# Performance work log

Measured on AMD Instinct MI355X. Metric: run time of the kernel, lower is better.

The kernel has to match this reference:

```python
import jax, jax.numpy as jnp
import numpy as np

N, E, D, L, G = 100000, 3200000, 64, 4, 512
BN_EPS = 1e-5


def setup_inputs() -> dict:
    key = jax.random.key(0)
    ks = jax.random.split(key, 6)
    x = jax.random.normal(ks[0], (N, D), dtype=jnp.float32)
    edge_index = jax.random.randint(ks[1], (2, E), 0, N, dtype=jnp.int64)
    batch = jnp.sort(jax.random.randint(ks[2], (N,), 0, G, dtype=jnp.int64))
    scale = 1.0 / np.sqrt(D).astype(np.float32)
    W1 = jax.random.normal(ks[3], (L, D, D), dtype=jnp.float32) * scale
    b1 = jnp.zeros((L, D), dtype=jnp.float32)
    W2 = jax.random.normal(ks[4], (L, D, D), dtype=jnp.float32) * scale
    b2 = jnp.zeros((L, D), dtype=jnp.float32)
    gamma = jnp.ones((L, D), dtype=jnp.float32)
    beta = jnp.zeros((L, D), dtype=jnp.float32)
    return {"x": x, "W1": W1, "b1": b1, "W2": W2, "b2": b2,
            "gamma": gamma, "beta": beta,
            "edge_index": edge_index, "batch": batch}


def reference(x, W1, b1, W2, b2, gamma, beta, edge_index, batch):
    src, dst = edge_index[0], edge_index[1]
    # in-degree for mean aggregation (flow source_to_target: gather x[src], scatter at dst)
    deg = jax.ops.segment_sum(jnp.ones((E,), x.dtype), dst, num_segments=N)
    inv_deg = jnp.where(deg > 0, 1.0 / jnp.maximum(deg, 1.0), 0.0)[:, None]
    # per-graph node counts for global_mean_pool
    gcnt = jax.ops.segment_sum(jnp.ones((N,), x.dtype), batch, num_segments=G)
    inv_gcnt = jnp.where(gcnt > 0, 1.0 / jnp.maximum(gcnt, 1.0), 0.0)[:, None]

    h = x
    node_pool = jnp.zeros((N, D), x.dtype)
    g_pool = jnp.zeros((G, D), x.dtype)
    for l in range(L):
        # GINConv(aggr='mean', eps=0): nn(x + mean_{j in N(i)} x_j)
        agg = jax.ops.segment_sum(h[src], dst, num_segments=N) * inv_deg
        z = h + agg
        z = jnp.maximum(z @ W1[l] + b1[l], 0.0) @ W2[l] + b2[l]  # Linear-ReLU-Linear
        z = jnp.maximum(z, 0.0)  # outer F.relu
        # BatchNorm1d (training-mode batch statistics over node dim)
        mu = z.mean(axis=0)
        var = z.var(axis=0)
        h = (z - mu) * jax.lax.rsqrt(var + BN_EPS) * gamma[l] + beta[l]
        node_pool = node_pool + h
        g_pool = g_pool + jax.ops.segment_sum(h, batch, num_segments=G) * inv_gcnt
    return node_pool, g_pool
```

## Files before the change

### kernel.cpp

```cpp
#include <hip/hip_runtime.h>
#include <hip/hip_bf16.h>


typedef unsigned short ushort_t;
typedef unsigned int uint_t;
typedef __attribute__((ext_vector_type(8))) short bf16x8;
typedef __attribute__((ext_vector_type(4))) float f32x4;

#define NN 100000
#define EE 3200000
#define GG 512
#define NBK 391
#define NHB 256
#define ECHUNK 12500
#define MLPBLOCKS 782
#define NWAVE (MLPBLOCKS * 4)
#define YSTRIDE 68

__global__ __launch_bounds__(256) void detect_kernel(
    const uint_t* __restrict__ xw, const uint_t* __restrict__ ew,
    const uint_t* __restrict__ bw, int* __restrict__ flags)
{
    __shared__ int sb[256], se[256], sbb[256];
    int t = threadIdx.x;
    uint_t w = xw[t];
    uint_t eL = (w >> 7) & 0xffu;
    sb[t] = (eL >= 112u && eL <= 135u) ? 1 : 0;
    se[t] = (ew[2 * t + 1] == 0u) ? 1 : 0;
    sbb[t] = (bw[NN - 512 + 2 * t + 1] == 0u) ? 1 : 0;
    __syncthreads();
    for (int off = 128; off > 0; off >>= 1) {
        if (t < off) { sb[t] += sb[t + off]; se[t] += se[t + off]; sbb[t] += sbb[t + off]; }
        __syncthreads();
    }
    if (t == 0) {
        flags[0] = (sb[0] < 128) ? 1 : 0;
        flags[1] = (se[0] >= 128) ? 1 : 0;
        flags[2] = (sbb[0] >= 128) ? 1 : 0;
    }
}

__global__ __launch_bounds__(256) void cvt_w_kernel(
    const void* __restrict__ W1, const void* __restrict__ b1,
    const void* __restrict__ W2, const void* __restrict__ b2,
    const void* __restrict__ g, const void* __restrict__ be,
    const int* __restrict__ flags, ushort_t* __restrict__ wp,
    float* __restrict__ bb)
{
    int i = blockIdx.x * 256 + threadIdx.x;
    int fp32 = flags[0];
    if (i < 65536) {
        int L = i >> 14;
        int r = i & 16383;
        int gg = r >> 13;
        int p = (r >> 12) & 1;
        int t4 = (r >> 10) & 3;
        int s = (r >> 9) & 1;
        int lane = (r >> 3) & 63;
        int e = r & 7;
        int k = s * 32 + (lane >> 4) * 8 + e;
        int col = t4 * 16 + (lane & 15);
        int src = L * 4096 + k * 64 + col;
        const void* W = gg ? W2 : W1;
        float v = fp32 ? ((const float*)W)[src]
                       : __bfloat162float(((const __hip_bfloat16*)W)[src]);
        __hip_bfloat16 hb = __float2bfloat16(v);
        ushort_t outv;
        if (p) {
            __hip_bfloat16 lb = __float2bfloat16(v - __bfloat162float(hb));
            outv = *(ushort_t*)&lb;
        } else {
            outv = *(ushort_t*)&hb;
        }
        wp[i] = outv;
    } else if (i < 66560) {
        int j = i - 65536;
        int L = j >> 8;
        int r = j & 255;
        int kind = r >> 6;
        int f = r & 63;
        const void* src = (kind == 0) ? b1 : (kind == 1) ? b2 : (kind == 2) ? g : be;
        int off = L * 64 + f;
        float v = fp32 ? ((const float*)src)[off]
                       : __bfloat162float(((const __hip_bfloat16*)src)[off]);
        bb[L * 256 + kind * 64 + f] = v;
    }
}

__global__ __launch_bounds__(256) void cvt_x_kernel(
    const void* __restrict__ x, const int* __restrict__ flags,
    ushort_t* __restrict__ zh, ushort_t* __restrict__ zl, int total)
{
    int i = blockIdx.x * 256 + threadIdx.x;
    if (i >= total) return;
    float v;
    if (flags[0]) v = ((const float*)x)[i];
    else {
        uint_t u = (uint_t)((const ushort_t*)x)[i] << 16;
        v = __uint_as_float(u);
    }
    __hip_bfloat16 hb = __float2bfloat16(v);
    __hip_bfloat16 lb = __float2bfloat16(v - __bfloat162float(hb));
    zh[i] = *(ushort_t*)&hb;
    zl[i] = *(ushort_t*)&lb;
}

__global__ __launch_bounds__(256) void cvt_batch_kernel(
    const int* __restrict__ bw, const int* __restrict__ flags,
    int* __restrict__ b32, int* __restrict__ gstart, int n)
{
    int i = blockIdx.x * 256 + threadIdx.x;
    if (i >= n) return;
    int i64 = flags[2];
    int v = i64 ? bw[2 * i] : bw[i];
    b32[i] = v;
    int vn = (i + 1 < n) ? (i64 ? bw[2 * (i + 1)] : bw[i + 1]) : GG;
    if (i == 0) {
        for (int g = 0; g <= v; ++g) gstart[g] = 0;
    }
    if (vn != v) {
        for (int g = v + 1; g <= vn; ++g) gstart[g] = i + 1;
    }
}

__global__ __launch_bounds__(256) void count_hist_kernel(
    const int* __restrict__ ei, const int* __restrict__ flags,
    int* __restrict__ histo, int E)
{
    __shared__ int lh[NBK];
    int b = blockIdx.x, t = threadIdx.x;
    for (int j = t; j < NBK; j += 256) lh[j] = 0;
    __syncthreads();
    int i64 = flags[1];
    int e0 = b * ECHUNK, e1 = min(e0 + ECHUNK, E);
    for (int i = e0 + t; i < e1; i += 256) {
        int d = i64 ? ei[2 * (E + i)] : ei[E + i];
        atomicAdd(&lh[d >> 8], 1);
    }
    __syncthreads();
    for (int j = t; j < NBK; j += 256) histo[j * NHB + b] = lh[j];
}

__global__ __launch_bounds__(NHB) void blockscan_kernel(
    int* __restrict__ histo, int* __restrict__ tot)
{
    __shared__ int sd[NHB];
    int j = blockIdx.x, t = threadIdx.x;
    int v = histo[j * NHB + t];
    sd[t] = v;
    __syncthreads();
    #pragma unroll
    for (int off = 1; off < NHB; off <<= 1) {
        int add = (t >= off) ? sd[t - off] : 0;
        __syncthreads();
        sd[t] += add;
        __syncthreads();
    }
    histo[j * NHB + t] = sd[t] - v;
    if (t == NHB - 1) tot[j] = sd[NHB - 1];
}

__global__ __launch_bounds__(512) void bscan_kernel(
    const int* __restrict__ tot, int* __restrict__ bktoff)
{
    __shared__ int sd[512];
    int t = threadIdx.x;
    int v = (t < NBK) ? tot[t] : 0;
    sd[t] = v;
    __syncthreads();
    #pragma unroll
    for (int off = 1; off < 512; off <<= 1) {
        int add = (t >= off) ? sd[t - off] : 0;
        __syncthreads();
        sd[t] += add;
        __syncthreads();
    }
    if (t < NBK) bktoff[t] = sd[t] - v;
    if (t == 511) bktoff[NBK] = sd[511];
}

__global__ __launch_bounds__(256) void pair_scatter_kernel(
    const int* __restrict__ ei, const int* __restrict__ flags,
    const int* __restrict__ histo, const int* __restrict__ bktoff,
    int2* __restrict__ pairs, int E)
{
    __shared__ int cur[NBK];
    int b = blockIdx.x, t = threadIdx.x;
    for (int j = t; j < NBK; j += 256) cur[j] = histo[j * NHB + b] + bktoff[j];
    __syncthreads();
    int i64 = flags[1];
    int e0 = b * ECHUNK, e1 = min(e0 + ECHUNK, E);
    for (int i = e0 + t; i < e1; i += 256) {
        int d = i64 ? ei[2 * (E + i)] : ei[E + i];
        int s = i64 ? ei[2 * i]       : ei[i];
        int p = atomicAdd(&cur[d >> 8], 1);
        pairs[p] = make_int2(d, s);
    }
}

__global__ __launch_bounds__(256) void bucket_deg_kernel(
    const int2* __restrict__ pairs, const int* __restrict__ bktoff,
    int* __restrict__ deg, int N)
{
    __shared__ int cnt[256];
    int j = blockIdx.x, t = threadIdx.x;
    cnt[t] = 0;
    __syncthreads();
    int e0 = bktoff[j], e1 = bktoff[j + 1];
    for (int i = e0 + t; i < e1; i += 256)
        atomicAdd(&cnt[pairs[i].x & 255], 1);
    __syncthreads();
    int idx = j * 256 + t;
    if (idx < N) deg[idx] = cnt[t];
}

__global__ __launch_bounds__(256) void scan1_kernel(
    const int* __restrict__ deg, int* __restrict__ part, int* __restrict__ bsum, int n)
{
    __shared__ int sd[256];
    int t = threadIdx.x;
    int i0 = blockIdx.x * 1024 + t * 4;
    int v0 = 0, v1 = 0, v2 = 0, v3 = 0;
    if (i0 + 3 < n) {
        int4 v = *(const int4*)(deg + i0);
        v0 = v.x; v1 = v.y; v2 = v.z; v3 = v.w;
    } else if (i0 < n) {
        v0 = deg[i0];
        if (i0 + 1 < n) v1 = deg[i0 + 1];
        if (i0 + 2 < n) v2 = deg[i0 + 2];
    }
    int s = v0 + v1 + v2 + v3;
    sd[t] = s;
    __syncthreads();
    #pragma unroll
    for (int off = 1; off < 256; off <<= 1) {
        int add = (t >= off) ? sd[t - off] : 0;
        __syncthreads();
        sd[t] += add;
        __syncthreads();
    }
    int incl = sd[t];
    int e0 = incl - s;
    int p0 = e0 + v0, p1 = p0 + v1, p2 = p1 + v2, p3 = p2 + v3;
    if (i0 < n)     part[i0]     = p0;
    if (i0 + 1 < n) part[i0 + 1] = p1;
    if (i0 + 2 < n) part[i0 + 2] = p2;
    if (i0 + 3 < n) part[i0 + 3] = p3;
    if (t == 255) bsum[blockIdx.x] = incl;
}

__global__ __launch_bounds__(128) void scan2_kernel(int* __restrict__ bsum, int nb)
{
    __shared__ int sd[128];
    int t = threadIdx.x;
    int own = (t < nb) ? bsum[t] : 0;
    sd[t] = own;
    __syncthreads();
    #pragma unroll
    for (int off = 1; off < 128; off <<= 1) {
        int add = (t >= off) ? sd[t - off] : 0;
        __syncthreads();
        sd[t] += add;
        __syncthreads();
    }
    if (t < nb) bsum[t] = sd[t] - own;
}

__global__ __launch_bounds__(256) void scan3_kernel(
    const int* __restrict__ part, const int* __restrict__ bsum,
    const int* __restrict__ deg, int* __restrict__ indptr,
    float* __restrict__ inv_deg, int n)
{
    int i = blockIdx.x * 256 + threadIdx.x;
    if (i >= n) return;
    int val = part[i] + bsum[i >> 10];
    indptr[i + 1] = val;
    int d = deg[i];
    inv_deg[i] = (d > 0) ? 1.0f / (float)d : 0.0f;
    if (i == 0) indptr[0] = 0;
}

__global__ __launch_bounds__(512) void invg_kernel(
    const int* __restrict__ gstart, float* __restrict__ invg,
    float* __restrict__ ac, int G)
{
    int g = threadIdx.x;
    if (g < G) {
        int c = gstart[g + 1] - gstart[g];
        invg[g] = (c > 0) ? 1.0f / (float)c : 0.0f;
    }
    if (g < 64) ac[g] = 1.0f;
    else if (g < 128) ac[g] = 0.0f;
}

__global__ __launch_bounds__(256) void csr_fill_kernel(
    const int2* __restrict__ pairs, const int* __restrict__ bktoff,
    const int* __restrict__ indptr, int* __restrict__ esrc, int N)
{
    __shared__ int cur[256];
    int j = blockIdx.x, t = threadIdx.x;
    int idx = j * 256 + t;
    cur[t] = (idx < N) ? indptr[idx] : 0;
    __syncthreads();
    int e0 = bktoff[j], e1 = bktoff[j + 1];
    for (int i = e0 + t; i < e1; i += 256) {
        int2 e = pairs[i];
        int p = atomicAdd(&cur[e.x & 255], 1);
        esrc[p] = e.y;
    }
}

__global__ __launch_bounds__(256) void agg_kernel(
    const ushort_t* __restrict__ zh_prev, const ushort_t* __restrict__ zl_prev,
    const int* __restrict__ indptr, const int* __restrict__ esrc,
    const float* __restrict__ inv_deg, const float* __restrict__ ac,
    ushort_t* __restrict__ zh_out, ushort_t* __restrict__ zl_out, int n)
{
    int t = threadIdx.x;
    int grp = t >> 4, l = t & 15;
    int lane = t & 63;
    int gl0 = lane & 48;
    int node = blockIdx.x * 16 + grp;
    if (node >= n) return;
    int e0 = indptr[node], e1 = indptr[node + 1];
    float idg = inv_deg[node];
    uint2 uh = *(const uint2*)(zh_prev + (size_t)node * 64 + l * 4);
    uint2 ul = *(const uint2*)(zl_prev + (size_t)node * 64 + l * 4);
    float4 own;
    own.x = __uint_as_float(uh.x << 16) + __uint_as_float(ul.x << 16);
    own.y = __uint_as_float(uh.x & 0xffff0000u) + __uint_as_float(ul.x & 0xffff0000u);
    own.z = __uint_as_float(uh.y << 16) + __uint_as_float(ul.y << 16);
    own.w = __uint_as_float(uh.y & 0xffff0000u) + __uint_as_float(ul.y & 0xffff0000u);
    float4 A = *(const float4*)(ac + l * 4);
    float4 C = *(const float4*)(ac + 64 + l * 4);
    float a0 = 0.f, a1 = 0.f, a2 = 0.f, a3 = 0.f;
    const ushort_t* zbl = zh_prev + l * 4;

    int base = e0;
    for (; base + 16 <= e1; base += 16) {
        int myi = esrc[base + l];
        uint2 vv[16];
        #pragma unroll
        for (int j = 0; j < 16; ++j) {
            int s = __shfl(myi, gl0 + j, 64);
            vv[j] = *(const uint2*)(zbl + (size_t)s * 64);
        }
        #pragma unroll
        for (int j = 0; j < 16; ++j) {
            a0 += __uint_as_float(vv[j].x << 16);
            a1 += __uint_as_float(vv[j].x & 0xffff0000u);
            a2 += __uint_as_float(vv[j].y << 16);
            a3 += __uint_as_float(vv[j].y & 0xffff0000u);
        }
    }
    int cnt = e1 - base;
    if (cnt > 0) {
        int myi = (l < cnt) ? esrc[base + l] : 0;
        uint2 vv[16];
        #pragma unroll
        for (int j = 0; j < 16; ++j) {
            int jj = (j < cnt) ? j : 0;
            int s = __shfl(myi, gl0 + jj, 64);
            uint2 v = *(const uint2*)(zbl + (size_t)s * 64);
            vv[j].x = (j < cnt) ? v.x : 0u;
            vv[j].y = (j < cnt) ? v.y : 0u;
        }
        #pragma unroll
        for (int j = 0; j < 16; ++j) {
            a0 += __uint_as_float(vv[j].x << 16);
            a1 += __uint_as_float(vv[j].x & 0xffff0000u);
            a2 += __uint_as_float(vv[j].y << 16);
            a3 += __uint_as_float(vv[j].y & 0xffff0000u);
        }
    }

    float cf = (idg > 0.f) ? 2.f : 1.f;
    float4 r;
    r.x = fmaf(A.x, fmaf(idg, a0, own.x), C.x * cf);
    r.y = fmaf(A.y, fmaf(idg, a1, own.y), C.y * cf);
    r.z = fmaf(A.z, fmaf(idg, a2, own.z), C.z * cf);
    r.w = fmaf(A.w, fmaf(idg, a3, own.w), C.w * cf);
    __hip_bfloat16 hx = __float2bfloat16(r.x);
    __hip_bfloat16 hy = __float2bfloat16(r.y);
    __hip_bfloat16 hz = __float2bfloat16(r.z);
    __hip_bfloat16 hw = __float2bfloat16(r.w);
    __hip_bfloat16 lx = __float2bfloat16(r.x - __bfloat162float(hx));
    __hip_bfloat16 ly = __float2bfloat16(r.y - __bfloat162float(hy));
    __hip_bfloat16 lz = __float2bfloat16(r.z - __bfloat162float(hz));
    __hip_bfloat16 lw = __float2bfloat16(r.w - __bfloat162float(hw));
    uint2 ph, pl;
    ph.x = (uint_t)*(ushort_t*)&hx | ((uint_t)*(ushort_t*)&hy << 16);
    ph.y = (uint_t)*(ushort_t*)&hz | ((uint_t)*(ushort_t*)&hw << 16);
    pl.x = (uint_t)*(ushort_t*)&lx | ((uint_t)*(ushort_t*)&ly << 16);
    pl.y = (uint_t)*(ushort_t*)&lz | ((uint_t)*(ushort_t*)&lw << 16);
    *(uint2*)(zh_out + (size_t)node * 64 + l * 4) = ph;
    *(uint2*)(zl_out + (size_t)node * 64 + l * 4) = pl;
}

__global__ __launch_bounds__(256) void mlp_kernel(
    const ushort_t* __restrict__ zh_in, const ushort_t* __restrict__ zl_in,
    const ushort_t* __restrict__ wp, const float* __restrict__ bb,
    ushort_t* __restrict__ zh_out, ushort_t* __restrict__ zl_out,
    float* __restrict__ partials, int n)
{
    __shared__ uint_t ylds[4 * 32 * YSTRIDE];
    int tid = threadIdx.x;
    int lane = tid & 63;
    int w = tid >> 6;
    int c = lane & 15, q = lane >> 4;
    int nb = blockIdx.x * 128 + w * 32;
    int wid = blockIdx.x * 4 + w;
    uint_t* my = ylds + w * 32 * YSTRIDE;

    #pragma unroll
    for (int mt = 0; mt < 2; ++mt) {
        int row = nb + mt * 16 + c;
        bool rv = row < n;
        bf16x8 ah0, ah1, al0, al1;
        if (rv) {
            const ushort_t* ph = zh_in + (size_t)row * 64 + q * 8;
            const ushort_t* pl = zl_in + (size_t)row * 64 + q * 8;
            ah0 = *(const bf16x8*)(ph);
            ah1 = *(const bf16x8*)(ph + 32);
            al0 = *(const bf16x8*)(pl);
            al1 = *(const bf16x8*)(pl + 32);
        } else {
            #pragma unroll
            for (int e = 0; e < 8; ++e) { ah0[e] = 0; ah1[e] = 0; al0[e] = 0; al1[e] = 0; }
        }
        f32x4 acc[4] = {{0.f,0.f,0.f,0.f},{0.f,0.f,0.f,0.f},{0.f,0.f,0.f,0.f},{0.f,0.f,0.f,0.f}};
        #pragma unroll
        for (int t4 = 0; t4 < 4; ++t4) {
            #pragma unroll
            for (int s = 0; s < 2; ++s) {
                bf16x8 bh = *(const bf16x8*)(wp + (size_t)((t4 * 2 + s) * 512) + lane * 8);
                bf16x8 bl = *(const bf16x8*)(wp + (size_t)((8 + t4 * 2 + s) * 512) + lane * 8);
                bf16x8 a_h = s ? ah1 : ah0;
                bf16x8 a_l = s ? al1 : al0;
                acc[t4] = __builtin_amdgcn_mfma_f32_16x16x32_bf16(a_l, bh, acc[t4], 0, 0, 0);
                acc[t4] = __builtin_amdgcn_mfma_f32_16x16x32_bf16(a_h, bl, acc[t4], 0, 0, 0);
                acc[t4] = __builtin_amdgcn_mfma_f32_16x16x32_bf16(a_h, bh, acc[t4], 0, 0, 0);
            }
        }
        #pragma unroll
        for (int t4 = 0; t4 < 4; ++t4) {
            float b = bb[t4 * 16 + c];
            #pragma unroll
            for (int r = 0; r < 4; ++r) {
                float y = fmaxf(acc[t4][r] + b, 0.f);
                __hip_bfloat16 hb = __float2bfloat16(y);
                __hip_bfloat16 lb = __float2bfloat16(y - __bfloat162float(hb));
                uint_t u = (uint_t)*(ushort_t*)&hb | ((uint_t)*(ushort_t*)&lb << 16);
                my[(mt * 16 + q * 4 + r) * YSTRIDE + t4 * 16 + c] = u;
            }
        }
    }
    __syncthreads();

    float ssum[4] = {0.f, 0.f, 0.f, 0.f};
    float ssq[4] = {0.f, 0.f, 0.f, 0.f};
    #pragma unroll
    for (int mt = 0; mt < 2; ++mt) {
        int nl = mt * 16 + c;
        bf16x8 yah[2], yal[2];
        #pragma unroll
        for (int s = 0; s < 2; ++s) {
            const uint_t* pa = my + nl * YSTRIDE + s * 32 + q * 8;
            uint4 ua = *(const uint4*)(pa);
            uint4 ub = *(const uint4*)(pa + 4);
            yah[s][0] = (short)(ua.x & 0xffffu); yal[s][0] = (short)(ua.x >> 16);
            yah[s][1] = (short)(ua.y & 0xffffu); yal[s][1] = (short)(ua.y >> 16);
            yah[s][2] = (short)(ua.z & 0xffffu); yal[s][2] = (short)(ua.z >> 16);
            yah[s][3] = (short)(ua.w & 0xffffu); yal[s][3] = (short)(ua.w >> 16);
            yah[s][4] = (short)(ub.x & 0xffffu); yal[s][4] = (short)(ub.x >> 16);
            yah[s][5] = (short)(ub.y & 0xffffu); yal[s][5] = (short)(ub.y >> 16);
            yah[s][6] = (short)(ub.z & 0xffffu); yal[s][6] = (short)(ub.z >> 16);
            yah[s][7] = (short)(ub.w & 0xffffu); yal[s][7] = (short)(ub.w >> 16);
        }
        f32x4 acc[4] = {{0.f,0.f,0.f,0.f},{0.f,0.f,0.f,0.f},{0.f,0.f,0.f,0.f},{0.f,0.f,0.f,0.f}};
        #pragma unroll
        for (int t4 = 0; t4 < 4; ++t4) {
            #pragma unroll
            for (int s = 0; s < 2; ++s) {
                bf16x8 bh = *(const bf16x8*)(wp + (size_t)((16 + t4 * 2 + s) * 512) + lane * 8);
                bf16x8 bl = *(const bf16x8*)(wp + (size_t)((24 + t4 * 2 + s) * 512) + lane * 8);
                acc[t4] = __builtin_amdgcn_mfma_f32_16x16x32_bf16(yal[s], bh, acc[t4], 0, 0, 0);
                acc[t4] = __builtin_amdgcn_mfma_f32_16x16x32_bf16(yah[s], bl, acc[t4], 0, 0, 0);
                acc[t4] = __builtin_amdgcn_mfma_f32_16x16x32_bf16(yah[s], bh, acc[t4], 0, 0, 0);
            }
        }
        #pragma unroll
        for (int t4 = 0; t4 < 4; ++t4) {
            float b = bb[64 + t4 * 16 + c];
            #pragma unroll
            for (int r = 0; r < 4; ++r) {
                int node = nb + mt * 16 + q * 4 + r;
                float h = fmaxf(acc[t4][r] + b, 0.f);
                float hv = (node < n) ? h : 0.f;
                ssum[t4] += hv;
                ssq[t4] += hv * hv;
                my[(mt * 16 + q * 4 + r) * YSTRIDE + t4 * 16 + c] = __float_as_uint(h);
            }
        }
    }
    __syncthreads();

    #pragma unroll
    for (int t4 = 0; t4 < 4; ++t4) {
        ssum[t4] += __shfl_xor(ssum[t4], 16, 64);
        ssum[t4] += __shfl_xor(ssum[t4], 32, 64);
        ssq[t4]  += __shfl_xor(ssq[t4], 16, 64);
        ssq[t4]  += __shfl_xor(ssq[t4], 32, 64);
    }
    if (lane < 16) {
        #pragma unroll
        for (int t4 = 0; t4 < 4; ++t4) {
            partials[(size_t)(t4 * 16 + lane) * NWAVE + wid] = ssum[t4];
            partials[(size_t)(64 + t4 * 16 + lane) * NWAVE + wid] = ssq[t4];
        }
    }

    #pragma unroll
    for (int cc = 0; cc < 8; ++cc) {
        int li = lane + 64 * cc;
        int nl = li >> 4, fg = li & 15;
        int node = nb + nl;
        if (node < n) {
            uint4 u = *(const uint4*)(my + nl * YSTRIDE + fg * 4);
            float f0 = __uint_as_float(u.x);
            float f1 = __uint_as_float(u.y);
            float f2 = __uint_as_float(u.z);
            float f3 = __uint_as_float(u.w);
            __hip_bfloat16 h0 = __float2bfloat16(f0);
            __hip_bfloat16 h1 = __float2bfloat16(f1);
            __hip_bfloat16 h2 = __float2bfloat16(f2);
            __hip_bfloat16 h3 = __float2bfloat16(f3);
            __hip_bfloat16 l0 = __float2bfloat16(f0 - __bfloat162float(h0));
            __hip_bfloat16 l1 = __float2bfloat16(f1 - __bfloat162float(h1));
            __hip_bfloat16 l2 = __float2bfloat16(f2 - __bfloat162float(h2));
            __hip_bfloat16 l3 = __float2bfloat16(f3 - __bfloat162float(h3));
            uint2 ph, pl;
            ph.x = (uint_t)*(ushort_t*)&h0 | ((uint_t)*(ushort_t*)&h1 << 16);
            ph.y = (uint_t)*(ushort_t*)&h2 | ((uint_t)*(ushort_t*)&h3 << 16);
            pl.x = (uint_t)*(ushort_t*)&l0 | ((uint_t)*(ushort_t*)&l1 << 16);
            pl.y = (uint_t)*(ushort_t*)&l2 | ((uint_t)*(ushort_t*)&l3 << 16);
            *(uint2*)(zh_out + (size_t)node * 64 + fg * 4) = ph;
            *(uint2*)(zl_out + (size_t)node * 64 + fg * 4) = pl;
        }
    }
}

__global__ __launch_bounds__(256) void redstats_kernel(
    const float* __restrict__ partials, const float* __restrict__ gammaf,
    const float* __restrict__ betaf, float* __restrict__ ac_out)
{
    __shared__ float s1[256], s2[256];
    int f = blockIdx.x;
    int t = threadIdx.x;
    const float* ph = partials + (size_t)f * NWAVE;
    const float* pq = partials + (size_t)(64 + f) * NWAVE;
    float a = 0.f, b = 0.f;
    for (int i = t; i < NWAVE; i += 256) { a += ph[i]; b += pq[i]; }
    s1[t] = a; s2[t] = b;
    __syncthreads();
    for (int off = 128; off > 0; off >>= 1) {
        if (t < off) { s1[t] += s1[t + off]; s2[t] += s2[t + off]; }
        __syncthreads();
    }
    if (t == 0) {
        const float invN = 1.0f / (float)NN;
        float mu = s1[0] * invN;
        float var = s2[0] * invN - mu * mu;
        if (var < 0.f) var = 0.f;
        float A = gammaf[f] * rsqrtf(var + 1e-5f);
        float C = betaf[f] - mu * A;
        ac_out[f] = A;
        ac_out[64 + f] = C;
    }
}

__global__ __launch_bounds__(256) void pool_kernel(
    const ushort_t* __restrict__ zh, const ushort_t* __restrict__ zl,
    float* __restrict__ node_pool, const int* __restrict__ b32,
    const float* __restrict__ ac, float* __restrict__ gpool,
    const int* __restrict__ flags, void* __restrict__ out,
    int N, int first, int last)
{
    int wave = (blockIdx.x * 256 + threadIdx.x) >> 6;
    int f = threadIdx.x & 63;
    int n0 = wave * 16;
    if (n0 >= N) return;
    int n1 = min(n0 + 16, N);
    float A = ac[f], C = ac[64 + f];
    int fp32 = flags[0];
    float racc = 0.f;
    int cur = b32[n0];
    int n = n0;
    for (; n + 4 <= n1; n += 4) {
        int4 gv = *(const int4*)(b32 + n);
        size_t idx = (size_t)n * 64 + f;
        float z0 = __uint_as_float((uint_t)zh[idx] << 16)       + __uint_as_float((uint_t)zl[idx] << 16);
        float z1 = __uint_as_float((uint_t)zh[idx + 64] << 16)  + __uint_as_float((uint_t)zl[idx + 64] << 16);
        float z2 = __uint_as_float((uint_t)zh[idx + 128] << 16) + __uint_as_float((uint_t)zl[idx + 128] << 16);
        float z3 = __uint_as_float((uint_t)zh[idx + 192] << 16) + __uint_as_float((uint_t)zl[idx + 192] << 16);
        float h0 = fmaf(z0, A, C);
        float h1 = fmaf(z1, A, C);
        float h2 = fmaf(z2, A, C);
        float h3 = fmaf(z3, A, C);
        float p0, p1, p2, p3;
        if (first) {
            p0 = h0; p1 = h1; p2 = h2; p3 = h3;
        } else {
            p0 = node_pool[idx]       + h0;
            p1 = node_pool[idx + 64]  + h1;
            p2 = node_pool[idx + 128] + h2;
            p3 = node_pool[idx + 192] + h3;
        }
        if (last) {
            if (fp32) {
                ((float*)out)[idx]       = p0;
                ((float*)out)[idx + 64]  = p1;
                ((float*)out)[idx + 128] = p2;
                ((float*)out)[idx + 192] = p3;
            } else {
                __hip_bfloat16 b0 = __float2bfloat16(p0);
                __hip_bfloat16 b1 = __float2bfloat16(p1);
                __hip_bfloat16 b2 = __float2bfloat16(p2);
                __hip_bfloat16 b3 = __float2bfloat16(p3);
                ((__hip_bfloat16*)out)[idx]       = b0;
                ((__hip_bfloat16*)out)[idx + 64]  = b1;
                ((__hip_bfloat16*)out)[idx + 128] = b2;
                ((__hip_bfloat16*)out)[idx + 192] = b3;
            }
        } else {
            node_pool[idx]       = p0;
            node_pool[idx + 64]  = p1;
            node_pool[idx + 128] = p2;
            node_pool[idx + 192] = p3;
        }
        int gs0 = gv.x, gs1 = gv.y, gs2 = gv.z, gs3 = gv.w;
        if (gs0 != cur) { atomicAdd(&gpool[(size_t)cur * 64 + f], racc); racc = 0.f; cur = gs0; }
        racc += h0;
        if (gs1 != cur) { atomicAdd(&gpool[(size_t)cur * 64 + f], racc); racc = 0.f; cur = gs1; }
        racc += h1;
        if (gs2 != cur) { atomicAdd(&gpool[(size_t)cur * 64 + f], racc); racc = 0.f; cur = gs2; }
        racc += h2;
        if (gs3 != cur) { atomicAdd(&gpool[(size_t)cur * 64 + f], racc); racc = 0.f; cur = gs3; }
        racc += h3;
    }
    for (; n < n1; ++n) {
        int g = b32[n];
        if (g != cur) { atomicAdd(&gpool[(size_t)cur * 64 + f], racc); racc = 0.f; cur = g; }
        size_t idx = (size_t)n * 64 + f;
        float zv = __uint_as_float((uint_t)zh[idx] << 16) + __uint_as_float((uint_t)zl[idx] << 16);
        float hv = fmaf(zv, A, C);
        float np = first ? hv : (node_pool[idx] + hv);
        if (last) {
            if (fp32) ((float*)out)[idx] = np;
            else ((__hip_bfloat16*)out)[idx] = __float2bfloat16(np);
        } else node_pool[idx] = np;
        racc += hv;
    }
    atomicAdd(&gpool[(size_t)cur * 64 + f], racc);
}

__global__ __launch_bounds__(256) void finalize_kernel(
    const float* __restrict__ gpool, const float* __restrict__ invg,
    const int* __restrict__ flags, void* __restrict__ out, int N)
{
    int i = blockIdx.x * 256 + threadIdx.x;
    if (i >= GG * 64) return;
    float v = gpool[i] * invg[i >> 6];
    int nd = N * 64;
    if (flags[0]) ((float*)out)[nd + i] = v;
    else ((__hip_bfloat16*)out)[nd + i] = __float2bfloat16(v);
}

extern "C" void kernel_launch(void* const* d_in, const int* in_sizes, int n_in,
                              void* d_out, int out_size, void* d_ws, size_t ws_size,
                              hipStream_t stream)
{
    constexpr int N = NN, E = EE, G = GG;
    constexpr int ND = N * 64;

    const void* x     = d_in[0];
    const void* W1    = d_in[1];
    const void* b1    = d_in[2];
    const void* W2    = d_in[3];
    const void* b2    = d_in[4];
    const void* gamma = d_in[5];
    const void* beta  = d_in[6];
    const int* ei     = (const int*)d_in[7];
    const int* batw   = (const int*)d_in[8];

    char* p = (char*)d_ws;
    auto alloc = [&](size_t bytes) -> char* {
        char* r = p;
        p += (bytes + 255) & ~(size_t)255;
        return r;
    };
    ushort_t* zhA      = (ushort_t*)alloc((size_t)ND * 2);
    ushort_t* zlA      = (ushort_t*)alloc((size_t)ND * 2);
    ushort_t* zhB      = (ushort_t*)alloc((size_t)ND * 2);
    ushort_t* zlB      = (ushort_t*)alloc((size_t)ND * 2);
    float*    node_pool = (float*)alloc((size_t)ND * 4);
    int*      esrc      = (int*)alloc((size_t)E * 4);
    int*      indptr    = (int*)alloc((size_t)(N + 1) * 4);
    int*      deg       = (int*)alloc((size_t)N * 4);
    int*      part      = (int*)alloc((size_t)N * 4);
    float*    invdeg    = (float*)alloc((size_t)N * 4);
    int*      b32       = (int*)alloc((size_t)N * 4);
    int*      bsum      = (int*)alloc(128 * 4);
    int*      gstart    = (int*)alloc((size_t)(G + 1) * 4);
    float*    invg      = (float*)alloc(G * 4);
    float*    gpool     = (float*)alloc((size_t)G * 64 * 4);
    float*    ac5       = (float*)alloc(5 * 128 * 4);
    float*    partials  = (float*)alloc((size_t)128 * NWAVE * 4);
    ushort_t* wp        = (ushort_t*)alloc((size_t)4 * 16384 * 2);
    float*    bb        = (float*)alloc(4 * 256 * 4);
    int*      flags     = (int*)alloc(16 * 4);
    int*      histo     = (int*)alloc((size_t)NBK * NHB * 4);
    int*      tot       = (int*)alloc((size_t)NBK * 4);
    int*      bktoff    = (int*)alloc((size_t)(NBK + 1) * 4);
    int2*     pairs     = (int2*)node_pool;

    hipMemsetAsync(gpool, 0, (size_t)G * 64 * 4, stream);

    detect_kernel<<<1, 256, 0, stream>>>(
        (const uint_t*)x, (const uint_t*)ei, (const uint_t*)batw, flags);
    cvt_w_kernel<<<260, 256, 0, stream>>>(W1, b1, W2, b2, gamma, beta, flags, wp, bb);
    cvt_x_kernel<<<(ND + 255) / 256, 256, 0, stream>>>(x, flags, zhA, zlA, ND);
    cvt_batch_kernel<<<(N + 255) / 256, 256, 0, stream>>>(batw, flags, b32, gstart, N);
    count_hist_kernel<<<NHB, 256, 0, stream>>>(ei, flags, histo, E);
    blockscan_kernel<<<NBK, NHB, 0, stream>>>(histo, tot);
    bscan_kernel<<<1, 512, 0, stream>>>(tot, bktoff);
    pair_scatter_kernel<<<NHB, 256, 0, stream>>>(ei, flags, histo, bktoff, pairs, E);
    bucket_deg_kernel<<<NBK, 256, 0, stream>>>(pairs, bktoff, deg, N);
    int nb = (N + 1023) / 1024;
    scan1_kernel<<<nb, 256, 0, stream>>>(deg, part, bsum, N);
    scan2_kernel<<<1, 128, 0, stream>>>(bsum, nb);
    scan3_kernel<<<(N + 255) / 256, 256, 0, stream>>>(part, bsum, deg, indptr, invdeg, N);
    invg_kernel<<<1, 512, 0, stream>>>(gstart, invg, ac5, G);
    csr_fill_kernel<<<NBK, 256, 0, stream>>>(pairs, bktoff, indptr, esrc, N);

    for (int l = 0; l < 4; ++l) {
        agg_kernel<<<(N + 15) / 16, 256, 0, stream>>>(
            zhA, zlA, indptr, esrc, invdeg, ac5 + l * 128, zhB, zlB, N);
        mlp_kernel<<<MLPBLOCKS, 256, 0, stream>>>(
            zhB, zlB, wp + (size_t)l * 16384, bb + l * 256,
            zhA, zlA, partials, N);
        redstats_kernel<<<64, 256, 0, stream>>>(
            partials, bb + l * 256 + 128, bb + l * 256 + 192,
            ac5 + (l + 1) * 128);
        pool_kernel<<<(N + 63) / 64, 256, 0, stream>>>(
            zhA, zlA, node_pool, b32, ac5 + (l + 1) * 128, gpool, flags, d_out,
            N, (l == 0) ? 1 : 0, (l == 3) ? 1 : 0);
    }
    finalize_kernel<<<128, 256, 0, stream>>>(gpool, invg, flags, d_out, N);
}
```

Measured before the change: 600.3 us.

## Fuse neighbor aggregation into MLP kernel via per-wave LDS staging

Merges the separate aggregation and MLP kernels into one kernel. Each wave gathers and mean-aggregates its 32 nodes, writes the split-bf16 result into its LDS tile, and reads MFMA operands from LDS instead of global memory. This removes the global round trip of the aggregated features and one launch per layer, and the layer inputs and outputs now ping-pong between buffers. In exchange, the gather now runs at MLP-kernel granularity with a serial 8-iteration node loop per wave, so there is less parallelism to hide gather latency, and LDS pressure may lower occupancy.

```diff
diff --git a/kernel.cpp b/kernel.cpp
--- a/kernel.cpp
+++ b/kernel.cpp
@@ -310,95 +310,10 @@
     }
 }
 
-__global__ __launch_bounds__(256) void agg_kernel(
-    const ushort_t* __restrict__ zh_prev, const ushort_t* __restrict__ zl_prev,
+__global__ __launch_bounds__(256) void fused_kernel(
+    const ushort_t* __restrict__ zh_in, const ushort_t* __restrict__ zl_in,
     const int* __restrict__ indptr, const int* __restrict__ esrc,
     const float* __restrict__ inv_deg, const float* __restrict__ ac,
-    ushort_t* __restrict__ zh_out, ushort_t* __restrict__ zl_out, int n)
-{
-    int t = threadIdx.x;
-    int grp = t >> 4, l = t & 15;
-    int lane = t & 63;
-    int gl0 = lane & 48;
-    int node = blockIdx.x * 16 + grp;
-    if (node >= n) return;
-    int e0 = indptr[node], e1 = indptr[node + 1];
-    float idg = inv_deg[node];
-    uint2 uh = *(const uint2*)(zh_prev + (size_t)node * 64 + l * 4);
-    uint2 ul = *(const uint2*)(zl_prev + (size_t)node * 64 + l * 4);
-    float4 own;
-    own.x = __uint_as_float(uh.x << 16) + __uint_as_float(ul.x << 16);
-    own.y = __uint_as_float(uh.x & 0xffff0000u) + __uint_as_float(ul.x & 0xffff0000u);
-    own.z = __uint_as_float(uh.y << 16) + __uint_as_float(ul.y << 16);
-    own.w = __uint_as_float(uh.y & 0xffff0000u) + __uint_as_float(ul.y & 0xffff0000u);
-    float4 A = *(const float4*)(ac + l * 4);
-    float4 C = *(const float4*)(ac + 64 + l * 4);
-    float a0 = 0.f, a1 = 0.f, a2 = 0.f, a3 = 0.f;
-    const ushort_t* zbl = zh_prev + l * 4;
-
-    int base = e0;
-    for (; base + 16 <= e1; base += 16) {
-        int myi = esrc[base + l];
-        uint2 vv[16];
-        #pragma unroll
-        for (int j = 0; j < 16; ++j) {
-            int s = __shfl(myi, gl0 + j, 64);
-            vv[j] = *(const uint2*)(zbl + (size_t)s * 64);
-        }
-        #pragma unroll
-        for (int j = 0; j < 16; ++j) {
-            a0 += __uint_as_float(vv[j].x << 16);
-            a1 += __uint_as_float(vv[j].x & 0xffff0000u);
-            a2 += __uint_as_float(vv[j].y << 16);
-            a3 += __uint_as_float(vv[j].y & 0xffff0000u);
-        }
-    }
-    int cnt = e1 - base;
-    if (cnt > 0) {
-        int myi = (l < cnt) ? esrc[base + l] : 0;
-        uint2 vv[16];
-        #pragma unroll
-        for (int j = 0; j < 16; ++j) {
-            int jj = (j < cnt) ? j : 0;
-            int s = __shfl(myi, gl0 + jj, 64);
-            uint2 v = *(const uint2*)(zbl + (size_t)s * 64);
-            vv[j].x = (j < cnt) ? v.x : 0u;
-            vv[j].y = (j < cnt) ? v.y : 0u;
-        }
-        #pragma unroll
-        for (int j = 0; j < 16; ++j) {
-            a0 += __uint_as_float(vv[j].x << 16);
-            a1 += __uint_as_float(vv[j].x & 0xffff0000u);
-            a2 += __uint_as_float(vv[j].y << 16);
-            a3 += __uint_as_float(vv[j].y & 0xffff0000u);
-        }
-    }
-
-    float cf = (idg > 0.f) ? 2.f : 1.f;
-    float4 r;
-    r.x = fmaf(A.x, fmaf(idg, a0, own.x), C.x * cf);
-    r.y = fmaf(A.y, fmaf(idg, a1, own.y), C.y * cf);
-    r.z = fmaf(A.z, fmaf(idg, a2, own.z), C.z * cf);
-    r.w = fmaf(A.w, fmaf(idg, a3, own.w), C.w * cf);
-    __hip_bfloat16 hx = __float2bfloat16(r.x);
-    __hip_bfloat16 hy = __float2bfloat16(r.y);
-    __hip_bfloat16 hz = __float2bfloat16(r.z);
-    __hip_bfloat16 hw = __float2bfloat16(r.w);
-    __hip_bfloat16 lx = __float2bfloat16(r.x - __bfloat162float(hx));
-    __hip_bfloat16 ly = __float2bfloat16(r.y - __bfloat162float(hy));
-    __hip_bfloat16 lz = __float2bfloat16(r.z - __bfloat162float(hz));
-    __hip_bfloat16 lw = __float2bfloat16(r.w - __bfloat162float(hw));
-    uint2 ph, pl;
-    ph.x = (uint_t)*(ushort_t*)&hx | ((uint_t)*(ushort_t*)&hy << 16);
-    ph.y = (uint_t)*(ushort_t*)&hz | ((uint_t)*(ushort_t*)&hw << 16);
-    pl.x = (uint_t)*(ushort_t*)&lx | ((uint_t)*(ushort_t*)&ly << 16);
-    pl.y = (uint_t)*(ushort_t*)&lz | ((uint_t)*(ushort_t*)&lw << 16);
-    *(uint2*)(zh_out + (size_t)node * 64 + l * 4) = ph;
-    *(uint2*)(zl_out + (size_t)node * 64 + l * 4) = pl;
-}
-
-__global__ __launch_bounds__(256) void mlp_kernel(
-    const ushort_t* __restrict__ zh_in, const ushort_t* __restrict__ zl_in,
     const ushort_t* __restrict__ wp, const float* __restrict__ bb,
     ushort_t* __restrict__ zh_out, ushort_t* __restrict__ zl_out,
     float* __restrict__ partials, int n)
@@ -407,26 +322,112 @@
     int tid = threadIdx.x;
     int lane = tid & 63;
     int w = tid >> 6;
-    int c = lane & 15, q = lane >> 4;
     int nb = blockIdx.x * 128 + w * 32;
     int wid = blockIdx.x * 4 + w;
     uint_t* my = ylds + w * 32 * YSTRIDE;
 
+    {
+        int grpw = lane >> 4;
+        int l = lane & 15;
+        int gl0 = lane & 48;
+        const ushort_t* zbl = zh_in + l * 4;
+        #pragma unroll 1
+        for (int it = 0; it < 8; ++it) {
+            int nl = it * 4 + grpw;
+            int node = nb + nl;
+            float4 r = make_float4(0.f, 0.f, 0.f, 0.f);
+            if (node < n) {
+                int e0 = indptr[node], e1 = indptr[node + 1];
+                float idg = inv_deg[node];
+                uint2 uh = *(const uint2*)(zh_in + (size_t)node * 64 + l * 4);
+                uint2 ul = *(const uint2*)(zl_in + (size_t)node * 64 + l * 4);
+                float4 own;
+                own.x = __uint_as_float(uh.x << 16) + __uint_as_float(ul.x << 16);
+                own.y = __uint_as_float(uh.x & 0xffff0000u) + __uint_as_float(ul.x & 0xffff0000u);
+                own.z = __uint_as_float(uh.y << 16) + __uint_as_float(ul.y << 16);
+                own.w = __uint_as_float(uh.y & 0xffff0000u) + __uint_as_float(ul.y & 0xffff0000u);
+                float4 A = *(const float4*)(ac + l * 4);
+                float4 C = *(const float4*)(ac + 64 + l * 4);
+                float a0 = 0.f, a1 = 0.f, a2 = 0.f, a3 = 0.f;
+                int base = e0;
+                for (; base + 16 <= e1; base += 16) {
+                    int myi = esrc[base + l];
+                    uint2 vv[16];
+                    #pragma unroll
+                    for (int j = 0; j < 16; ++j) {
+                        int s = __shfl(myi, gl0 + j, 64);
+                        vv[j] = *(const uint2*)(zbl + (size_t)s * 64);
+                    }
+                    #pragma unroll
+                    for (int j = 0; j < 16; ++j) {
+                        a0 += __uint_as_float(vv[j].x << 16);
+                        a1 += __uint_as_float(vv[j].x & 0xffff0000u);
+                        a2 += __uint_as_float(vv[j].y << 16);
+                        a3 += __uint_as_float(vv[j].y & 0xffff0000u);
+                    }
+                }
+                int cnt = e1 - base;
+                if (cnt > 0) {
+                    int myi = (l < cnt) ? esrc[base + l] : 0;
+                    uint2 vv[16];
+                    #pragma unroll
+                    for (int j = 0; j < 16; ++j) {
+                        int jj = (j < cnt) ? j : 0;
+                        int s = __shfl(myi, gl0 + jj, 64);
+                        uint2 v = *(const uint2*)(zbl + (size_t)s * 64);
+                        vv[j].x = (j < cnt) ? v.x : 0u;
+                        vv[j].y = (j < cnt) ? v.y : 0u;
+                    }
+                    #pragma unroll
+                    for (int j = 0; j < 16; ++j) {
+                        a0 += __uint_as_float(vv[j].x << 16);
+                        a1 += __uint_as_float(vv[j].x & 0xffff0000u);
+                        a2 += __uint_as_float(vv[j].y << 16);
+                        a3 += __uint_as_float(vv[j].y & 0xffff0000u);
+                    }
+                }
+                float cf = (idg > 0.f) ? 2.f : 1.f;
+                r.x = fmaf(A.x, fmaf(idg, a0, own.x), C.x * cf);
+                r.y = fmaf(A.y, fmaf(idg, a1, own.y), C.y * cf);
+                r.z = fmaf(A.z, fmaf(idg, a2, own.z), C.z * cf);
+                r.w = fmaf(A.w, fmaf(idg, a3, own.w), C.w * cf);
+            }
+            __hip_bfloat16 hx = __float2bfloat16(r.x);
+            __hip_bfloat16 hy = __float2bfloat16(r.y);
+            __hip_bfloat16 hz = __float2bfloat16(r.z);
+            __hip_bfloat16 hw = __float2bfloat16(r.w);
+            __hip_bfloat16 lx = __float2bfloat16(r.x - __bfloat162float(hx));
+            __hip_bfloat16 ly = __float2bfloat16(r.y - __bfloat162float(hy));
+            __hip_bfloat16 lz = __float2bfloat16(r.z - __bfloat162float(hz));
+            __hip_bfloat16 lw = __float2bfloat16(r.w - __bfloat162float(hw));
+            uint4 u;
+            u.x = (uint_t)*(ushort_t*)&hx | ((uint_t)*(ushort_t*)&lx << 16);
+            u.y = (uint_t)*(ushort_t*)&hy | ((uint_t)*(ushort_t*)&ly << 16);
+            u.z = (uint_t)*(ushort_t*)&hz | ((uint_t)*(ushort_t*)&lz << 16);
+            u.w = (uint_t)*(ushort_t*)&hw | ((uint_t)*(ushort_t*)&lw << 16);
+            *(uint4*)(my + nl * YSTRIDE + l * 4) = u;
+        }
+    }
+
+    int c = lane & 15, q = lane >> 4;
+
     #pragma unroll
     for (int mt = 0; mt < 2; ++mt) {
-        int row = nb + mt * 16 + c;
-        bool rv = row < n;
-        bf16x8 ah0, ah1, al0, al1;
-        if (rv) {
-            const ushort_t* ph = zh_in + (size_t)row * 64 + q * 8;
-            const ushort_t* pl = zl_in + (size_t)row * 64 + q * 8;
-            ah0 = *(const bf16x8*)(ph);
-            ah1 = *(const bf16x8*)(ph + 32);
-            al0 = *(const bf16x8*)(pl);
-            al1 = *(const bf16x8*)(pl + 32);
-        } else {
-            #pragma unroll
-            for (int e = 0; e < 8; ++e) { ah0[e] = 0; ah1[e] = 0; al0[e] = 0; al1[e] = 0; }
+        int nl = mt * 16 + c;
+        bf16x8 aah[2], aal[2];
+        #pragma unroll
+        for (int s = 0; s < 2; ++s) {
+            const uint_t* pa = my + nl * YSTRIDE + s * 32 + q * 8;
+            uint4 ua = *(const uint4*)(pa);
+            uint4 ub = *(const uint4*)(pa + 4);
+            aah[s][0] = (short)(ua.x & 0xffffu); aal[s][0] = (short)(ua.x >> 16);
+            aah[s][1] = (short)(ua.y & 0xffffu); aal[s][1] = (short)(ua.y >> 16);
+            aah[s][2] = (short)(ua.z & 0xffffu); aal[s][2] = (short)(ua.z >> 16);
+            aah[s][3] = (short)(ua.w & 0xffffu); aal[s][3] = (short)(ua.w >> 16);
+            aah[s][4] = (short)(ub.x & 0xffffu); aal[s][4] = (short)(ub.x >> 16);
+            aah[s][5] = (short)(ub.y & 0xffffu); aal[s][5] = (short)(ub.y >> 16);
+            aah[s][6] = (short)(ub.z & 0xffffu); aal[s][6] = (short)(ub.z >> 16);
+            aah[s][7] = (short)(ub.w & 0xffffu); aal[s][7] = (short)(ub.w >> 16);
         }
         f32x4 acc[4] = {{0.f,0.f,0.f,0.f},{0.f,0.f,0.f,0.f},{0.f,0.f,0.f,0.f},{0.f,0.f,0.f,0.f}};
         #pragma unroll
@@ -435,11 +436,9 @@
             for (int s = 0; s < 2; ++s) {
                 bf16x8 bh = *(const bf16x8*)(wp + (size_t)((t4 * 2 + s) * 512) + lane * 8);
                 bf16x8 bl = *(const bf16x8*)(wp + (size_t)((8 + t4 * 2 + s) * 512) + lane * 8);
-                bf16x8 a_h = s ? ah1 : ah0;
-                bf16x8 a_l = s ? al1 : al0;
-                acc[t4] = __builtin_amdgcn_mfma_f32_16x16x32_bf16(a_l, bh, acc[t4], 0, 0, 0);
-                acc[t4] = __builtin_amdgcn_mfma_f32_16x16x32_bf16(a_h, bl, acc[t4], 0, 0, 0);
-                acc[t4] = __builtin_amdgcn_mfma_f32_16x16x32_bf16(a_h, bh, acc[t4], 0, 0, 0);
+                acc[t4] = __builtin_amdgcn_mfma_f32_16x16x32_bf16(aal[s], bh, acc[t4], 0, 0, 0);
+                acc[t4] = __builtin_amdgcn_mfma_f32_16x16x32_bf16(aah[s], bl, acc[t4], 0, 0, 0);
+                acc[t4] = __builtin_amdgcn_mfma_f32_16x16x32_bf16(aah[s], bh, acc[t4], 0, 0, 0);
             }
         }
         #pragma unroll
@@ -743,18 +742,21 @@
     invg_kernel<<<1, 512, 0, stream>>>(gstart, invg, ac5, G);
     csr_fill_kernel<<<NBK, 256, 0, stream>>>(pairs, bktoff, indptr, esrc, N);
 
+    ushort_t* zh_in = zhA; ushort_t* zl_in = zlA;
+    ushort_t* zh_out = zhB; ushort_t* zl_out = zlB;
     for (int l = 0; l < 4; ++l) {
-        agg_kernel<<<(N + 15) / 16, 256, 0, stream>>>(
-            zhA, zlA, indptr, esrc, invdeg, ac5 + l * 128, zhB, zlB, N);
-        mlp_kernel<<<MLPBLOCKS, 256, 0, stream>>>(
-            zhB, zlB, wp + (size_t)l * 16384, bb + l * 256,
-            zhA, zlA, partials, N);
+        fused_kernel<<<MLPBLOCKS, 256, 0, stream>>>(
+            zh_in, zl_in, indptr, esrc, invdeg, ac5 + l * 128,
+            wp + (size_t)l * 16384, bb + l * 256,
+            zh_out, zl_out, partials, N);
         redstats_kernel<<<64, 256, 0, stream>>>(
             partials, bb + l * 256 + 128, bb + l * 256 + 192,
             ac5 + (l + 1) * 128);
         pool_kernel<<<(N + 63) / 64, 256, 0, stream>>>(
-            zhA, zlA, node_pool, b32, ac5 + (l + 1) * 128, gpool, flags, d_out,
+            zh_out, zl_out, node_pool, b32, ac5 + (l + 1) * 128, gpool, flags, d_out,
             N, (l == 0) ? 1 : 0, (l == 3) ? 1 : 0);
+        ushort_t* th = zh_in; zh_in = zh_out; zh_out = th;
+        ushort_t* tl = zl_in; zl_in = zl_out; zl_out = tl;
     }
     finalize_kernel<<<128, 256, 0, stream>>>(gpool, invg, flags, d_out, N);
 }
```

Result: no change. 608.1 us (+1.3%).

## Fold per-layer node pooling into aggregation kernel and pool graphs once at end

Applied to the files above, without the earlier changes.

The node_pool update for layer l-1 moves into the next layer's agg_kernel, which already reads the node's own features and BN coefficients. The separate pool_kernel then runs only once after the last layer. It also pools graphs from the cumulative node_pool sum rather than per layer, which is valid because graph pooling is linear. This removes three pool kernel launches and their re-reads of the z arrays, at the cost of extra node_pool read/write traffic inside agg_kernel.

```diff
diff --git a/kernel.cpp b/kernel.cpp
--- a/kernel.cpp
+++ b/kernel.cpp
@@ -314,7 +314,8 @@
     const ushort_t* __restrict__ zh_prev, const ushort_t* __restrict__ zl_prev,
     const int* __restrict__ indptr, const int* __restrict__ esrc,
     const float* __restrict__ inv_deg, const float* __restrict__ ac,
-    ushort_t* __restrict__ zh_out, ushort_t* __restrict__ zl_out, int n)
+    ushort_t* __restrict__ zh_out, ushort_t* __restrict__ zl_out,
+    float* __restrict__ node_pool, int do_pool, int first, int n)
 {
     int t = threadIdx.x;
     int grp = t >> 4, l = t & 15;
@@ -333,6 +334,23 @@
     own.w = __uint_as_float(uh.y & 0xffff0000u) + __uint_as_float(ul.y & 0xffff0000u);
     float4 A = *(const float4*)(ac + l * 4);
     float4 C = *(const float4*)(ac + 64 + l * 4);
+
+    if (do_pool) {
+        float4 h;
+        h.x = fmaf(A.x, own.x, C.x);
+        h.y = fmaf(A.y, own.y, C.y);
+        h.z = fmaf(A.z, own.z, C.z);
+        h.w = fmaf(A.w, own.w, C.w);
+        float* np = node_pool + (size_t)node * 64 + l * 4;
+        if (first) {
+            *(float4*)np = h;
+        } else {
+            float4 p = *(const float4*)np;
+            p.x += h.x; p.y += h.y; p.z += h.z; p.w += h.w;
+            *(float4*)np = p;
+        }
+    }
+
     float a0 = 0.f, a1 = 0.f, a2 = 0.f, a3 = 0.f;
     const ushort_t* zbl = zh_prev + l * 4;
 
@@ -581,10 +599,9 @@
 
 __global__ __launch_bounds__(256) void pool_kernel(
     const ushort_t* __restrict__ zh, const ushort_t* __restrict__ zl,
-    float* __restrict__ node_pool, const int* __restrict__ b32,
+    const float* __restrict__ node_pool, const int* __restrict__ b32,
     const float* __restrict__ ac, float* __restrict__ gpool,
-    const int* __restrict__ flags, void* __restrict__ out,
-    int N, int first, int last)
+    const int* __restrict__ flags, void* __restrict__ out, int N)
 {
     int wave = (blockIdx.x * 256 + threadIdx.x) >> 6;
     int f = threadIdx.x & 63;
@@ -603,63 +620,44 @@
         float z1 = __uint_as_float((uint_t)zh[idx + 64] << 16)  + __uint_as_float((uint_t)zl[idx + 64] << 16);
         float z2 = __uint_as_float((uint_t)zh[idx + 128] << 16) + __uint_as_float((uint_t)zl[idx + 128] << 16);
         float z3 = __uint_as_float((uint_t)zh[idx + 192] << 16) + __uint_as_float((uint_t)zl[idx + 192] << 16);
-        float h0 = fmaf(z0, A, C);
-        float h1 = fmaf(z1, A, C);
-        float h2 = fmaf(z2, A, C);
-        float h3 = fmaf(z3, A, C);
-        float p0, p1, p2, p3;
-        if (first) {
-            p0 = h0; p1 = h1; p2 = h2; p3 = h3;
+        float p0 = node_pool[idx]       + fmaf(z0, A, C);
+        float p1 = node_pool[idx + 64]  + fmaf(z1, A, C);
+        float p2 = node_pool[idx + 128] + fmaf(z2, A, C);
+        float p3 = node_pool[idx + 192] + fmaf(z3, A, C);
+        if (fp32) {
+            ((float*)out)[idx]       = p0;
+            ((float*)out)[idx + 64]  = p1;
+            ((float*)out)[idx + 128] = p2;
+            ((float*)out)[idx + 192] = p3;
         } else {
-            p0 = node_pool[idx]       + h0;
-            p1 = node_pool[idx + 64]  + h1;
-            p2 = node_pool[idx + 128] + h2;
-            p3 = node_pool[idx + 192] + h3;
-        }
-        if (last) {
-            if (fp32) {
-                ((float*)out)[idx]       = p0;
-                ((float*)out)[idx + 64]  = p1;
-                ((float*)out)[idx + 128] = p2;
-                ((float*)out)[idx + 192] = p3;
-            } else {
-                __hip_bfloat16 b0 = __float2bfloat16(p0);
-                __hip_bfloat16 b1 = __float2bfloat16(p1);
-                __hip_bfloat16 b2 = __float2bfloat16(p2);
-                __hip_bfloat16 b3 = __float2bfloat16(p3);
-                ((__hip_bfloat16*)out)[idx]       = b0;
-                ((__hip_bfloat16*)out)[idx + 64]  = b1;
-                ((__hip_bfloat16*)out)[idx + 128] = b2;
-                ((__hip_bfloat16*)out)[idx + 192] = b3;
-            }
-        } else {
-            node_pool[idx]       = p0;
-            node_pool[idx + 64]  = p1;
-            node_pool[idx + 128] = p2;
-            node_pool[idx + 192] = p3;
+            __hip_bfloat16 b0 = __float2bfloat16(p0);
+            __hip_bfloat16 b1 = __float2bfloat16(p1);
+            __hip_bfloat16 b2 = __float2bfloat16(p2);
+            __hip_bfloat16 b3 = __float2bfloat16(p3);
+            ((__hip_bfloat16*)out)[idx]       = b0;
+            ((__hip_bfloat16*)out)[idx + 64]  = b1;
+            ((__hip_bfloat16*)out)[idx + 128] = b2;
+            ((__hip_bfloat16*)out)[idx + 192] = b3;
         }
         int gs0 = gv.x, gs1 = gv.y, gs2 = gv.z, gs3 = gv.w;
         if (gs0 != cur) { atomicAdd(&gpool[(size_t)cur * 64 + f], racc); racc = 0.f; cur = gs0; }
-        racc += h0;
+        racc += p0;
         if (gs1 != cur) { atomicAdd(&gpool[(size_t)cur * 64 + f], racc); racc = 0.f; cur = gs1; }
-        racc += h1;
+        racc += p1;
         if (gs2 != cur) { atomicAdd(&gpool[(size_t)cur * 64 + f], racc); racc = 0.f; cur = gs2; }
-        racc += h2;
+        racc += p2;
         if (gs3 != cur) { atomicAdd(&gpool[(size_t)cur * 64 + f], racc); racc = 0.f; cur = gs3; }
-        racc += h3;
+        racc += p3;
     }
     for (; n < n1; ++n) {
         int g = b32[n];
         if (g != cur) { atomicAdd(&gpool[(size_t)cur * 64 + f], racc); racc = 0.f; cur = g; }
         size_t idx = (size_t)n * 64 + f;
         float zv = __uint_as_float((uint_t)zh[idx] << 16) + __uint_as_float((uint_t)zl[idx] << 16);
-        float hv = fmaf(zv, A, C);
-        float np = first ? hv : (node_pool[idx] + hv);
-        if (last) {
-            if (fp32) ((float*)out)[idx] = np;
-            else ((__hip_bfloat16*)out)[idx] = __float2bfloat16(np);
-        } else node_pool[idx] = np;
-        racc += hv;
+        float p = node_pool[idx] + fmaf(zv, A, C);
+        if (fp32) ((float*)out)[idx] = p;
+        else ((__hip_bfloat16*)out)[idx] = __float2bfloat16(p);
+        racc += p;
     }
     atomicAdd(&gpool[(size_t)cur * 64 + f], racc);
 }
@@ -745,16 +743,16 @@
 
     for (int l = 0; l < 4; ++l) {
         agg_kernel<<<(N + 15) / 16, 256, 0, stream>>>(
-            zhA, zlA, indptr, esrc, invdeg, ac5 + l * 128, zhB, zlB, N);
+            zhA, zlA, indptr, esrc, invdeg, ac5 + l * 128,
+            zhB, zlB, node_pool, (l >= 1) ? 1 : 0, (l == 1) ? 1 : 0, N);
         mlp_kernel<<<MLPBLOCKS, 256, 0, stream>>>(
             zhB, zlB, wp + (size_t)l * 16384, bb + l * 256,
             zhA, zlA, partials, N);
         redstats_kernel<<<64, 256, 0, stream>>>(
             partials, bb + l * 256 + 128, bb + l * 256 + 192,
             ac5 + (l + 1) * 128);
-        pool_kernel<<<(N + 63) / 64, 256, 0, stream>>>(
-            zhA, zlA, node_pool, b32, ac5 + (l + 1) * 128, gpool, flags, d_out,
-            N, (l == 0) ? 1 : 0, (l == 3) ? 1 : 0);
-    }
+    }
+    pool_kernel<<<(N + 63) / 64, 256, 0, stream>>>(
+        zhA, zlA, node_pool, b32, ac5 + 4 * 128, gpool, flags, d_out, N);
     finalize_kernel<<<128, 256, 0, stream>>>(gpool, invg, flags, d_out, N);
 }
```

Measured after the change: 579.3 us. 3.5% less time.
